# Performance work log

Measured on AMD Instinct MI355X. Metric: run time of the kernel, lower is better.

## Reference

```python
import jax, jax.numpy as jnp
import numpy as np

INPUT_DIM = 512
HIDDEN_DIM = 512
B, N = 8, 2048


def setup_inputs() -> dict:
    key = jax.random.key(0)
    ks = jax.random.split(key, 9)
    s_in = 1.0 / np.sqrt(INPUT_DIM)
    s_h = 1.0 / np.sqrt(HIDDEN_DIM)
    return {
        "X": jax.random.normal(ks[0], (B, N, INPUT_DIM), dtype=jnp.float32),
        "Wq": jax.random.uniform(ks[1], (INPUT_DIM, HIDDEN_DIM), minval=-s_in, maxval=s_in),
        "bq": jnp.zeros((HIDDEN_DIM,), jnp.float32),
        "Wk": jax.random.uniform(ks[2], (INPUT_DIM, HIDDEN_DIM), minval=-s_in, maxval=s_in),
        "bk": jnp.zeros((HIDDEN_DIM,), jnp.float32),
        "Wv": jax.random.uniform(ks[3], (INPUT_DIM, HIDDEN_DIM), minval=-s_in, maxval=s_in),
        "bv": jnp.zeros((HIDDEN_DIM,), jnp.float32),
        "Wo": jax.random.uniform(ks[4], (HIDDEN_DIM, INPUT_DIM), minval=-s_h, maxval=s_h),
        "bo": jnp.zeros((INPUT_DIM,), jnp.float32),
        "ln_gamma": jnp.ones((INPUT_DIM,), jnp.float32),
        "ln_beta": jnp.zeros((INPUT_DIM,), jnp.float32),
    }


def reference(X, Wq, bq, Wk, bk, Wv, bv, Wo, bo, ln_gamma, ln_beta):
    q = X @ Wq + bq                      # [B,N,H]
    k = X @ Wk + bk
    v = X @ Wv + bv
    scores = jnp.einsum('bnh,bmh->bnm', q, k) / jnp.sqrt(jnp.float32(HIDDEN_DIM))
    attn = jax.nn.softmax(scores, axis=-1)      # [B,N,N]
    ctx = jnp.einsum('bnm,bmh->bnh', attn, v)   # [B,N,H]
    out = ctx @ Wo + bo + X                      # residual
    mu = jnp.mean(out, axis=-1, keepdims=True)
    var = jnp.var(out, axis=-1, keepdims=True)
    normed = (out - mu) / jnp.sqrt(var + 1e-5)
    return normed * ln_gamma + ln_beta
```

## Files before the change

### kernel.cpp

```cpp
#include <hip/hip_runtime.h>
#include <cstdint>
#include <cstddef>


typedef __bf16 bf16x8 __attribute__((ext_vector_type(8)));
typedef float  f32x4  __attribute__((ext_vector_type(4)));

__device__ __forceinline__ uint16_t f2bf(float f) {
  union { float f; uint32_t u; } v; v.f = f;
  uint32_t r = v.u + 0x7FFFu + ((v.u >> 16) & 1u);
  return (uint16_t)(r >> 16);
}

__device__ __forceinline__ void gld16(const uint16_t* g, uint16_t* l) {
  __builtin_amdgcn_global_load_lds(
      (__attribute__((address_space(1))) void*)(g),
      (__attribute__((address_space(3))) void*)(l), 16, 0, 0);
}

template <int MODE, int BM, int BN>
__global__ __launch_bounds__(256, 2) void gemm_k(
    const uint16_t* __restrict__ A, const uint16_t* __restrict__ Bt,
    void* __restrict__ OutA, uint16_t* __restrict__ OutK,
    uint16_t* __restrict__ OutVT, float* __restrict__ rsum, int K, int lda,
    int ldb, const float* __restrict__ b0, const float* __restrict__ b1,
    const float* __restrict__ b2, const float* __restrict__ Xres, float scale) {
  constexpr int MT = BM / 32;
  constexpr int NT = BN / 32;
  constexpr int AI = BM / 64;
  constexpr int BI = BN / 64;
  __shared__ alignas(16) uint16_t As[2 * BM * 32];
  __shared__ alignas(16) uint16_t Bs[2 * BN * 32];

  const int tid = threadIdx.x;
  const int w = tid >> 6, lane = tid & 63;
  const int wm = w >> 1, wn = w & 1;
  const int m0 = blockIdx.y * BM, n0 = blockIdx.x * BN;
  const int z = blockIdx.z;

  const uint16_t* Ab = A;
  const uint16_t* Bb = Bt;
  if (MODE == 1) { Ab += (size_t)z * 2048 * 512;  Bb += (size_t)z * 2048 * 512; }
  if (MODE == 2) { Ab += (size_t)z * 2048 * 2048; Bb += (size_t)z * 512 * 2048; }

  const int kc = (lane & 3) * 8;
  const int rbaseA = w * (BM / 4);
  const int rbaseB = w * (BN / 4);
  const uint16_t* gA = Ab + (size_t)(m0 + rbaseA + (lane >> 2)) * lda + kc;
  const uint16_t* gB = Bb + (size_t)(n0 + rbaseB + (lane >> 2)) * ldb + kc;
  uint16_t* lA0 = &As[rbaseA * 32];
  uint16_t* lB0 = &Bs[rbaseB * 32];

  f32x4 acc[MT][NT];
#pragma unroll
  for (int i = 0; i < MT; i++)
#pragma unroll
    for (int j = 0; j < NT; j++) acc[i][j] = (f32x4){0.f, 0.f, 0.f, 0.f};

  const int lr = lane & 15;
  const int q8 = (lane >> 4) * 8;

  for (int k0 = 0; k0 < K; k0 += 64) {
#pragma unroll
    for (int h = 0; h < 2; h++) {
#pragma unroll
      for (int j = 0; j < AI; j++)
        gld16(gA + k0 + h * 32 + (size_t)(j * 16) * lda,
              lA0 + h * BM * 32 + j * 16 * 32);
#pragma unroll
      for (int j = 0; j < BI; j++)
        gld16(gB + k0 + h * 32 + (size_t)(j * 16) * ldb,
              lB0 + h * BN * 32 + j * 16 * 32);
    }
    __syncthreads();
#pragma unroll
    for (int h = 0; h < 2; h++) {
      bf16x8 af[MT], bfr[NT];
#pragma unroll
      for (int t = 0; t < MT; t++)
        af[t] = *(const bf16x8*)
            &As[h * BM * 32 + (wm * (BM / 2) + t * 16 + lr) * 32 + q8];
#pragma unroll
      for (int t = 0; t < NT; t++)
        bfr[t] = *(const bf16x8*)
            &Bs[h * BN * 32 + (wn * (BN / 2) + t * 16 + lr) * 32 + q8];
#pragma unroll
      for (int nt = 0; nt < NT; nt++)
#pragma unroll
        for (int mt = 0; mt < MT; mt++)
          acc[mt][nt] = __builtin_amdgcn_mfma_f32_16x16x32_bf16(
              af[mt], bfr[nt], acc[mt][nt], 0, 0, 0);
    }
    __syncthreads();
  }

  if (MODE == 1) {
    uint16_t* Sp = (uint16_t*)OutA + (size_t)z * 2048 * 2048;
#pragma unroll
    for (int mt = 0; mt < MT; mt++) {
      float rp[4] = {0.f, 0.f, 0.f, 0.f};
#pragma unroll
      for (int nt = 0; nt < NT; nt++) {
#pragma unroll
        for (int i = 0; i < 4; i++) {
          const int row = m0 + wm * (BM / 2) + mt * 16 + (lane >> 4) * 4 + i;
          const int col = n0 + wn * (BN / 2) + nt * 16 + lr;
          const float e = __expf(acc[mt][nt][i] * scale);
          Sp[(size_t)row * 2048 + col] = f2bf(e);
          rp[i] += e;
        }
      }
#pragma unroll
      for (int i = 0; i < 4; i++) {
        float p = rp[i];
        p += __shfl_xor(p, 1); p += __shfl_xor(p, 2);
        p += __shfl_xor(p, 4); p += __shfl_xor(p, 8);
        if (lr == 0) {
          const int row = m0 + wm * (BM / 2) + mt * 16 + (lane >> 4) * 4 + i;
          atomicAdd(&rsum[z * 2048 + row], p);
        }
      }
    }
  } else if (MODE == 2) {
#pragma unroll
    for (int mt = 0; mt < MT; mt++) {
#pragma unroll
      for (int i = 0; i < 4; i++) {
        const int row = m0 + wm * (BM / 2) + mt * 16 + (lane >> 4) * 4 + i;
        const float sc = 1.0f / rsum[z * 2048 + row];
#pragma unroll
        for (int nt = 0; nt < NT; nt++) {
          const int col = n0 + wn * (BN / 2) + nt * 16 + lr;
          ((uint16_t*)OutA)[((size_t)z * 2048 + row) * 512 + col] =
              f2bf(acc[mt][nt][i] * sc);
        }
      }
    }
  } else {
#pragma unroll
    for (int mt = 0; mt < MT; mt++) {
#pragma unroll
      for (int nt = 0; nt < NT; nt++) {
#pragma unroll
        for (int i = 0; i < 4; i++) {
          const int row = m0 + wm * (BM / 2) + mt * 16 + (lane >> 4) * 4 + i;
          const int col = n0 + wn * (BN / 2) + nt * 16 + lr;
          const float v = acc[mt][nt][i];
          if (MODE == 0) {
            const int which = col >> 9, c = col & 511;
            if (which == 0) {
              ((uint16_t*)OutA)[(size_t)row * 512 + c] = f2bf(v + b0[c]);
            } else if (which == 1) {
              OutK[(size_t)row * 512 + c] = f2bf(v + b1[c]);
            } else {
              OutVT[(size_t)(row >> 11) * (512 * 2048) + (size_t)c * 2048 +
                    (row & 2047)] = f2bf(v + b2[c]);
            }
          } else {
            const size_t idx = (size_t)row * 512 + col;
            ((float*)OutA)[idx] = v + b0[col] + Xres[idx];
          }
        }
      }
    }
  }
}

__global__ __launch_bounds__(256) void cvt_all_k(
    const float* __restrict__ X, uint16_t* __restrict__ Xb,
    const float* __restrict__ Wq, const float* __restrict__ Wk,
    const float* __restrict__ Wv, const float* __restrict__ Wo,
    uint16_t* __restrict__ Wt, float* __restrict__ rsum) {
  const int i = blockIdx.x * 256 + threadIdx.x;
  const float4 f = ((const float4*)X)[i];
  uint32_t lo = (uint32_t)f2bf(f.x) | ((uint32_t)f2bf(f.y) << 16);
  uint32_t hi = (uint32_t)f2bf(f.z) | ((uint32_t)f2bf(f.w) << 16);
  ((uint2*)Xb)[i] = make_uint2(lo, hi);
  if (i < 16384) rsum[i] = 0.f;
  if (i < 2048 * 512) {
    const int n = i >> 9, kk = i & 511;
    const int which = n >> 9, c = n & 511;
    const float* W =
        (which == 0) ? Wq : (which == 1) ? Wk : (which == 2) ? Wv : Wo;
    Wt[i] = f2bf(W[kk * 512 + c]);
  }
}

__global__ __launch_bounds__(256) void ln_k(float* __restrict__ O,
                                            const float* __restrict__ g,
                                            const float* __restrict__ b) {
  const int tid = threadIdx.x, w = tid >> 6, lane = tid & 63;
  float* p = O + ((size_t)blockIdx.x * 4 + w) * 512;
  float4 v0 = ((const float4*)p)[lane];
  float4 v1 = ((const float4*)p)[64 + lane];
  float s  = v0.x + v0.y + v0.z + v0.w + v1.x + v1.y + v1.z + v1.w;
  float sq = v0.x * v0.x + v0.y * v0.y + v0.z * v0.z + v0.w * v0.w +
             v1.x * v1.x + v1.y * v1.y + v1.z * v1.z + v1.w * v1.w;
#pragma unroll
  for (int off = 32; off >= 1; off >>= 1) {
    s += __shfl_xor(s, off);
    sq += __shfl_xor(sq, off);
  }
  const float mean = s * (1.f / 512.f);
  const float var = sq * (1.f / 512.f) - mean * mean;
  const float rstd = rsqrtf(var + 1e-5f);
  const float4 g0 = ((const float4*)g)[lane], g1 = ((const float4*)g)[64 + lane];
  const float4 b0 = ((const float4*)b)[lane], b1 = ((const float4*)b)[64 + lane];
  v0.x = (v0.x - mean) * rstd * g0.x + b0.x;
  v0.y = (v0.y - mean) * rstd * g0.y + b0.y;
  v0.z = (v0.z - mean) * rstd * g0.z + b0.z;
  v0.w = (v0.w - mean) * rstd * g0.w + b0.w;
  v1.x = (v1.x - mean) * rstd * g1.x + b1.x;
  v1.y = (v1.y - mean) * rstd * g1.y + b1.y;
  v1.z = (v1.z - mean) * rstd * g1.z + b1.z;
  v1.w = (v1.w - mean) * rstd * g1.w + b1.w;
  ((float4*)p)[lane] = v0;
  ((float4*)p)[64 + lane] = v1;
}

extern "C" void kernel_launch(void* const* d_in, const int* in_sizes, int n_in,
                              void* d_out, int out_size, void* d_ws,
                              size_t ws_size, hipStream_t stream) {
  const float* X     = (const float*)d_in[0];
  const float* Wq    = (const float*)d_in[1];
  const float* bq    = (const float*)d_in[2];
  const float* Wk    = (const float*)d_in[3];
  const float* bk    = (const float*)d_in[4];
  const float* Wv    = (const float*)d_in[5];
  const float* bv    = (const float*)d_in[6];
  const float* Wo    = (const float*)d_in[7];
  const float* bo    = (const float*)d_in[8];
  const float* gamma = (const float*)d_in[9];
  const float* beta  = (const float*)d_in[10];
  float* out = (float*)d_out;

  char* ws = (char*)d_ws;
  uint16_t* S    = (uint16_t*)(ws);
  uint16_t* Xb   = (uint16_t*)(ws);
  uint16_t* Wt   = (uint16_t*)(ws + 67108864);
  uint16_t* q    = (uint16_t*)(ws + 69206016);
  uint16_t* kb   = (uint16_t*)(ws + 85983232);
  uint16_t* vT   = (uint16_t*)(ws + 102760448);
  float*    rsum = (float*)(ws + 119537664);
  uint16_t* ctx  = q;

  cvt_all_k<<<dim3(8192), dim3(256), 0, stream>>>(X, Xb, Wq, Wk, Wv, Wo, Wt,
                                                  rsum);
  gemm_k<0, 128, 256><<<dim3(6, 128, 1), dim3(256), 0, stream>>>(
      Xb, Wt, (void*)q, kb, vT, nullptr, 512, 512, 512, bq, bk, bv, nullptr,
      1.f);
  gemm_k<1, 128, 256><<<dim3(8, 16, 8), dim3(256), 0, stream>>>(
      q, kb, (void*)S, nullptr, nullptr, rsum, 512, 512, 512, nullptr, nullptr,
      nullptr, nullptr, 0.044194173824159216f);
  gemm_k<2, 64, 256><<<dim3(2, 32, 8), dim3(256), 0, stream>>>(
      S, vT, (void*)ctx, nullptr, nullptr, rsum, 2048, 2048, 2048, nullptr,
      nullptr, nullptr, nullptr, 1.f);
  gemm_k<3, 128, 128><<<dim3(4, 128, 1), dim3(256), 0, stream>>>(
      ctx, Wt + 1536 * 512, (void*)out, nullptr, nullptr, nullptr, 512, 512,
      512, bo, nullptr, nullptr, X, 1.f);
  ln_k<<<dim3(4096), dim3(256), 0, stream>>>(out, gamma, beta);
}
```

Before: 348.3 us.

## Pipeline GEMM K-loop with triple-buffered LDS and async prefetch

Replaces the load-then-compute K loop, which had two barriers per 64-wide step, with a 3-stage ring of 32-wide LDS buffers. Global-to-LDS loads run two stages ahead, guarded by vmcnt waits and a single barrier per step, so memory latency overlaps with MFMA work. The BN tile for the QKV, score and PV GEMMs drops from 256 to 128 to fit the extra buffer and raise block count. This costs smaller per-block reuse and more grid blocks, and relies on the hand-written vmcnt counting being exact.

```diff
diff --git a/kernel.cpp b/kernel.cpp
--- a/kernel.cpp
+++ b/kernel.cpp
@@ -29,8 +29,9 @@
   constexpr int NT = BN / 32;
   constexpr int AI = BM / 64;
   constexpr int BI = BN / 64;
-  __shared__ alignas(16) uint16_t As[2 * BM * 32];
-  __shared__ alignas(16) uint16_t Bs[2 * BN * 32];
+  constexpr int PW = AI + BI;
+  __shared__ alignas(16) uint16_t As[3][BM * 32];
+  __shared__ alignas(16) uint16_t Bs[3][BN * 32];
 
   const int tid = threadIdx.x;
   const int w = tid >> 6, lane = tid & 63;
@@ -44,12 +45,10 @@
   if (MODE == 2) { Ab += (size_t)z * 2048 * 2048; Bb += (size_t)z * 512 * 2048; }
 
   const int kc = (lane & 3) * 8;
-  const int rbaseA = w * (BM / 4);
-  const int rbaseB = w * (BN / 4);
-  const uint16_t* gA = Ab + (size_t)(m0 + rbaseA + (lane >> 2)) * lda + kc;
-  const uint16_t* gB = Bb + (size_t)(n0 + rbaseB + (lane >> 2)) * ldb + kc;
-  uint16_t* lA0 = &As[rbaseA * 32];
-  uint16_t* lB0 = &Bs[rbaseB * 32];
+  const int rbA = w * (BM / 4);
+  const int rbB = w * (BN / 4);
+  const uint16_t* gA = Ab + (size_t)(m0 + rbA + (lane >> 2)) * lda + kc;
+  const uint16_t* gB = Bb + (size_t)(n0 + rbB + (lane >> 2)) * ldb + kc;
 
   f32x4 acc[MT][NT];
 #pragma unroll
@@ -59,40 +58,47 @@
 
   const int lr = lane & 15;
   const int q8 = (lane >> 4) * 8;
-
-  for (int k0 = 0; k0 < K; k0 += 64) {
-#pragma unroll
-    for (int h = 0; h < 2; h++) {
-#pragma unroll
-      for (int j = 0; j < AI; j++)
-        gld16(gA + k0 + h * 32 + (size_t)(j * 16) * lda,
-              lA0 + h * BM * 32 + j * 16 * 32);
-#pragma unroll
-      for (int j = 0; j < BI; j++)
-        gld16(gB + k0 + h * 32 + (size_t)(j * 16) * ldb,
-              lB0 + h * BN * 32 + j * 16 * 32);
-    }
-    __syncthreads();
-#pragma unroll
-    for (int h = 0; h < 2; h++) {
-      bf16x8 af[MT], bfr[NT];
-#pragma unroll
-      for (int t = 0; t < MT; t++)
-        af[t] = *(const bf16x8*)
-            &As[h * BM * 32 + (wm * (BM / 2) + t * 16 + lr) * 32 + q8];
-#pragma unroll
-      for (int t = 0; t < NT; t++)
-        bfr[t] = *(const bf16x8*)
-            &Bs[h * BN * 32 + (wn * (BN / 2) + t * 16 + lr) * 32 + q8];
-#pragma unroll
-      for (int nt = 0; nt < NT; nt++)
-#pragma unroll
-        for (int mt = 0; mt < MT; mt++)
-          acc[mt][nt] = __builtin_amdgcn_mfma_f32_16x16x32_bf16(
-              af[mt], bfr[nt], acc[mt][nt], 0, 0, 0);
-    }
-    __syncthreads();
-  }
+  const int iters = K >> 5;
+
+  auto stage = [&](int t, int buf) {
+    const int k0 = t * 32;
+#pragma unroll
+    for (int j = 0; j < AI; j++)
+      gld16(gA + k0 + (size_t)(j * 16) * lda, &As[buf][(rbA + j * 16) * 32]);
+#pragma unroll
+    for (int j = 0; j < BI; j++)
+      gld16(gB + k0 + (size_t)(j * 16) * ldb, &Bs[buf][(rbB + j * 16) * 32]);
+  };
+
+  auto compute = [&](int buf) {
+    bf16x8 af[MT], bfr[NT];
+#pragma unroll
+    for (int t = 0; t < MT; t++)
+      af[t] = *(const bf16x8*)&As[buf][(wm * (BM / 2) + t * 16 + lr) * 32 + q8];
+#pragma unroll
+    for (int t = 0; t < NT; t++)
+      bfr[t] = *(const bf16x8*)&Bs[buf][(wn * (BN / 2) + t * 16 + lr) * 32 + q8];
+#pragma unroll
+    for (int nt = 0; nt < NT; nt++)
+#pragma unroll
+      for (int mt = 0; mt < MT; mt++)
+        acc[mt][nt] = __builtin_amdgcn_mfma_f32_16x16x32_bf16(
+            af[mt], bfr[nt], acc[mt][nt], 0, 0, 0);
+  };
+
+  stage(0, 0);
+  stage(1, 1);
+  int buf = 0;
+  for (int i = 0; i < iters - 1; ++i) {
+    asm volatile("s_waitcnt vmcnt(%0)" ::"i"(PW) : "memory");
+    __builtin_amdgcn_s_barrier();
+    if (i + 2 < iters) stage(i + 2, (buf + 2 >= 3) ? buf - 1 : buf + 2);
+    compute(buf);
+    buf = (buf == 2) ? 0 : buf + 1;
+  }
+  asm volatile("s_waitcnt vmcnt(0)" ::: "memory");
+  __builtin_amdgcn_s_barrier();
+  compute(buf);
 
   if (MODE == 1) {
     uint16_t* Sp = (uint16_t*)OutA + (size_t)z * 2048 * 2048;
@@ -246,13 +252,13 @@
 
   cvt_all_k<<<dim3(8192), dim3(256), 0, stream>>>(X, Xb, Wq, Wk, Wv, Wo, Wt,
                                                   rsum);
-  gemm_k<0, 128, 256><<<dim3(6, 128, 1), dim3(256), 0, stream>>>(
+  gemm_k<0, 128, 128><<<dim3(12, 128, 1), dim3(256), 0, stream>>>(
       Xb, Wt, (void*)q, kb, vT, nullptr, 512, 512, 512, bq, bk, bv, nullptr,
       1.f);
-  gemm_k<1, 128, 256><<<dim3(8, 16, 8), dim3(256), 0, stream>>>(
+  gemm_k<1, 128, 128><<<dim3(16, 16, 8), dim3(256), 0, stream>>>(
       q, kb, (void*)S, nullptr, nullptr, rsum, 512, 512, 512, nullptr, nullptr,
       nullptr, nullptr, 0.044194173824159216f);
-  gemm_k<2, 64, 256><<<dim3(2, 32, 8), dim3(256), 0, stream>>>(
+  gemm_k<2, 64, 128><<<dim3(4, 32, 8), dim3(256), 0, stream>>>(
       S, vT, (void*)ctx, nullptr, nullptr, rsum, 2048, 2048, 2048, nullptr,
       nullptr, nullptr, nullptr, 1.f);
   gemm_k<3, 128, 128><<<dim3(4, 128, 1), dim3(256), 0, stream>>>(
```

Result: faster. 327.9 us (-5.9%).

## Load MFMA fragments directly from global memory, dropping LDS staging

Applied to the files above, without the earlier changes.

The GEMM kernel no longer stages A/B tiles through shared memory with global_load_lds and barriers. Each wave now loads its bf16x8 MFMA fragments straight from global memory inside an unrolled compile-time K loop. Tile sizes shrink (BN 256→128) and launch-bound occupancy hints rise, giving more blocks. This removes LDS traffic and __syncthreads, but gives up cross-wave data reuse, so global/L2 traffic rises and the uncoalesced 16-byte row-strided loads may cost more.

```diff
diff --git a/kernel.cpp b/kernel.cpp
--- a/kernel.cpp
+++ b/kernel.cpp
@@ -12,25 +12,15 @@
   return (uint16_t)(r >> 16);
 }
 
-__device__ __forceinline__ void gld16(const uint16_t* g, uint16_t* l) {
-  __builtin_amdgcn_global_load_lds(
-      (__attribute__((address_space(1))) void*)(g),
-      (__attribute__((address_space(3))) void*)(l), 16, 0, 0);
-}
-
-template <int MODE, int BM, int BN>
-__global__ __launch_bounds__(256, 2) void gemm_k(
+template <int MODE, int BM, int BN, int KK, int MINW>
+__global__ __launch_bounds__(256, MINW) void gemm_k(
     const uint16_t* __restrict__ A, const uint16_t* __restrict__ Bt,
     void* __restrict__ OutA, uint16_t* __restrict__ OutK,
-    uint16_t* __restrict__ OutVT, float* __restrict__ rsum, int K, int lda,
-    int ldb, const float* __restrict__ b0, const float* __restrict__ b1,
+    uint16_t* __restrict__ OutVT, float* __restrict__ rsum, int lda, int ldb,
+    const float* __restrict__ b0, const float* __restrict__ b1,
     const float* __restrict__ b2, const float* __restrict__ Xres, float scale) {
   constexpr int MT = BM / 32;
   constexpr int NT = BN / 32;
-  constexpr int AI = BM / 64;
-  constexpr int BI = BN / 64;
-  __shared__ alignas(16) uint16_t As[2 * BM * 32];
-  __shared__ alignas(16) uint16_t Bs[2 * BN * 32];
 
   const int tid = threadIdx.x;
   const int w = tid >> 6, lane = tid & 63;
@@ -43,55 +33,37 @@
   if (MODE == 1) { Ab += (size_t)z * 2048 * 512;  Bb += (size_t)z * 2048 * 512; }
   if (MODE == 2) { Ab += (size_t)z * 2048 * 2048; Bb += (size_t)z * 512 * 2048; }
 
-  const int kc = (lane & 3) * 8;
-  const int rbaseA = w * (BM / 4);
-  const int rbaseB = w * (BN / 4);
-  const uint16_t* gA = Ab + (size_t)(m0 + rbaseA + (lane >> 2)) * lda + kc;
-  const uint16_t* gB = Bb + (size_t)(n0 + rbaseB + (lane >> 2)) * ldb + kc;
-  uint16_t* lA0 = &As[rbaseA * 32];
-  uint16_t* lB0 = &Bs[rbaseB * 32];
-
-  f32x4 acc[MT][NT];
-#pragma unroll
-  for (int i = 0; i < MT; i++)
-#pragma unroll
-    for (int j = 0; j < NT; j++) acc[i][j] = (f32x4){0.f, 0.f, 0.f, 0.f};
-
   const int lr = lane & 15;
   const int q8 = (lane >> 4) * 8;
 
-  for (int k0 = 0; k0 < K; k0 += 64) {
-#pragma unroll
-    for (int h = 0; h < 2; h++) {
-#pragma unroll
-      for (int j = 0; j < AI; j++)
-        gld16(gA + k0 + h * 32 + (size_t)(j * 16) * lda,
-              lA0 + h * BM * 32 + j * 16 * 32);
-#pragma unroll
-      for (int j = 0; j < BI; j++)
-        gld16(gB + k0 + h * 32 + (size_t)(j * 16) * ldb,
-              lB0 + h * BN * 32 + j * 16 * 32);
-    }
-    __syncthreads();
-#pragma unroll
-    for (int h = 0; h < 2; h++) {
-      bf16x8 af[MT], bfr[NT];
-#pragma unroll
-      for (int t = 0; t < MT; t++)
-        af[t] = *(const bf16x8*)
-            &As[h * BM * 32 + (wm * (BM / 2) + t * 16 + lr) * 32 + q8];
-#pragma unroll
-      for (int t = 0; t < NT; t++)
-        bfr[t] = *(const bf16x8*)
-            &Bs[h * BN * 32 + (wn * (BN / 2) + t * 16 + lr) * 32 + q8];
-#pragma unroll
-      for (int nt = 0; nt < NT; nt++)
-#pragma unroll
-        for (int mt = 0; mt < MT; mt++)
-          acc[mt][nt] = __builtin_amdgcn_mfma_f32_16x16x32_bf16(
-              af[mt], bfr[nt], acc[mt][nt], 0, 0, 0);
-    }
-    __syncthreads();
+  const uint16_t* aP[MT];
+  const uint16_t* bP[NT];
+#pragma unroll
+  for (int t = 0; t < MT; t++)
+    aP[t] = Ab + (size_t)(m0 + wm * (BM / 2) + t * 16 + lr) * lda + q8;
+#pragma unroll
+  for (int t = 0; t < NT; t++)
+    bP[t] = Bb + (size_t)(n0 + wn * (BN / 2) + t * 16 + lr) * ldb + q8;
+
+  f32x4 acc[MT][NT];
+#pragma unroll
+  for (int i = 0; i < MT; i++)
+#pragma unroll
+    for (int j = 0; j < NT; j++) acc[i][j] = (f32x4){0.f, 0.f, 0.f, 0.f};
+
+#pragma unroll 4
+  for (int k0 = 0; k0 < KK; k0 += 32) {
+    bf16x8 af[MT], bfr[NT];
+#pragma unroll
+    for (int t = 0; t < MT; t++) af[t] = *(const bf16x8*)(aP[t] + k0);
+#pragma unroll
+    for (int t = 0; t < NT; t++) bfr[t] = *(const bf16x8*)(bP[t] + k0);
+#pragma unroll
+    for (int nt = 0; nt < NT; nt++)
+#pragma unroll
+      for (int mt = 0; mt < MT; mt++)
+        acc[mt][nt] = __builtin_amdgcn_mfma_f32_16x16x32_bf16(
+            af[mt], bfr[nt], acc[mt][nt], 0, 0, 0);
   }
 
   if (MODE == 1) {
@@ -246,17 +218,16 @@
 
   cvt_all_k<<<dim3(8192), dim3(256), 0, stream>>>(X, Xb, Wq, Wk, Wv, Wo, Wt,
                                                   rsum);
-  gemm_k<0, 128, 256><<<dim3(6, 128, 1), dim3(256), 0, stream>>>(
-      Xb, Wt, (void*)q, kb, vT, nullptr, 512, 512, 512, bq, bk, bv, nullptr,
-      1.f);
-  gemm_k<1, 128, 256><<<dim3(8, 16, 8), dim3(256), 0, stream>>>(
-      q, kb, (void*)S, nullptr, nullptr, rsum, 512, 512, 512, nullptr, nullptr,
+  gemm_k<0, 128, 128, 512, 3><<<dim3(12, 128, 1), dim3(256), 0, stream>>>(
+      Xb, Wt, (void*)q, kb, vT, nullptr, 512, 512, bq, bk, bv, nullptr, 1.f);
+  gemm_k<1, 128, 128, 512, 3><<<dim3(16, 16, 8), dim3(256), 0, stream>>>(
+      q, kb, (void*)S, nullptr, nullptr, rsum, 512, 512, nullptr, nullptr,
       nullptr, nullptr, 0.044194173824159216f);
-  gemm_k<2, 64, 256><<<dim3(2, 32, 8), dim3(256), 0, stream>>>(
-      S, vT, (void*)ctx, nullptr, nullptr, rsum, 2048, 2048, 2048, nullptr,
-      nullptr, nullptr, nullptr, 1.f);
-  gemm_k<3, 128, 128><<<dim3(4, 128, 1), dim3(256), 0, stream>>>(
+  gemm_k<2, 64, 128, 2048, 4><<<dim3(4, 32, 8), dim3(256), 0, stream>>>(
+      S, vT, (void*)ctx, nullptr, nullptr, rsum, 2048, 2048, nullptr, nullptr,
+      nullptr, nullptr, 1.f);
+  gemm_k<3, 128, 128, 512, 3><<<dim3(4, 128, 1), dim3(256), 0, stream>>>(
       ctx, Wt + 1536 * 512, (void*)out, nullptr, nullptr, nullptr, 512, 512,
-      512, bo, nullptr, nullptr, X, 1.f);
+      bo, nullptr, nullptr, X, 1.f);
   ln_k<<<dim3(4096), dim3(256), 0, stream>>>(out, gamma, beta);
 }
```

New measurement: 605.3 us. 1.74x slower.
